# Optimization experiments

Measured on AMD Instinct MI355X. Metric: run time of the kernel, lower is better.

## Reference

```python
import jax, jax.numpy as jnp
import numpy as np

N_NODES = 50000
N_EDGES = 800000
IN_C, OUT_C, EDGE_F, HEADS, HID, FINAL = 8, 16, 8, 4, 64, 128
NEG_SLOPE = 0.2  # PyG GATConv default LeakyReLU slope


def setup_inputs() -> dict:
    key = jax.random.key(0)
    ks = jax.random.split(key, 12)
    s = 0.1
    return {
        "x": jax.random.normal(ks[0], (N_NODES, IN_C), jnp.float32),
        "edge_index": jax.random.randint(ks[1], (2, N_EDGES), 0, N_NODES, jnp.int64),
        "edge_attr": jax.random.normal(ks[2], (N_EDGES, EDGE_F), jnp.float32),
        # NNConv params: root weight, bias, edge-MLP Linear(EDGE_F -> IN_C*OUT_C)
        "ecc_root": jax.random.normal(ks[3], (IN_C, OUT_C), jnp.float32) * s,
        "ecc_bias": jnp.zeros((OUT_C,), jnp.float32),
        "mlp_w": jax.random.normal(ks[4], (EDGE_F, IN_C * OUT_C), jnp.float32) * s,
        "mlp_b": jnp.zeros((IN_C * OUT_C,), jnp.float32),
        # GATConv params
        "gat_lin": jax.random.normal(ks[5], (OUT_C, HEADS * HID), jnp.float32) * s,
        "att_src": jax.random.normal(ks[6], (HEADS, HID), jnp.float32) * s,
        "att_dst": jax.random.normal(ks[7], (HEADS, HID), jnp.float32) * s,
        "gat_bias": jnp.zeros((HEADS * HID,), jnp.float32),
        # final Linear
        "fc_w": jax.random.normal(ks[8], (HEADS * HID, FINAL), jnp.float32) * s,
        "fc_b": jnp.zeros((FINAL,), jnp.float32),
    }


def _forward(x, edge_index, edge_attr, ecc_root, ecc_bias, mlp_w, mlp_b,
             gat_lin, att_src, att_dst, gat_bias, fc_w, fc_b):
    src, dst = edge_index[0], edge_index[1]  # messages flow src -> dst

    # ---- NNConv (edge-conditioned conv), aggr='add' ----
    # per-edge weight matrices [E, IN_C, OUT_C] from edge MLP
    w_e = (edge_attr @ mlp_w + mlp_b).reshape(-1, IN_C, OUT_C)
    msg = jnp.einsum('ei,eio->eo', x[src], w_e)                 # [E, OUT_C]
    agg = jax.ops.segment_sum(msg, dst, num_segments=N_NODES)   # [N, OUT_C]
    h = jax.nn.relu(x @ ecc_root + agg + ecc_bias)              # [N, OUT_C]

    # ---- GATConv (heads concatenated) ----
    g = (h @ gat_lin).reshape(N_NODES, HEADS, HID)              # [N, H, D]
    a_src = jnp.einsum('nhd,hd->nh', g, att_src)                # [N, H]
    a_dst = jnp.einsum('nhd,hd->nh', g, att_dst)
    e = jax.nn.leaky_relu(a_src[src] + a_dst[dst], NEG_SLOPE)   # [E, H]
    # segment softmax over incoming edges of each dst node
    e_max = jax.ops.segment_max(e, dst, num_segments=N_NODES)   # [N, H]
    e_max = jnp.where(jnp.isfinite(e_max), e_max, 0.0)
    e_exp = jnp.exp(e - e_max[dst])                             # [E, H]
    denom = jax.ops.segment_sum(e_exp, dst, num_segments=N_NODES)
    alpha = e_exp / (denom[dst] + 1e-16)                        # [E, H]
    out = jax.ops.segment_sum(alpha[:, :, None] * g[src], dst,
                              num_segments=N_NODES)             # [N, H, D]
    out = jax.nn.relu(out.reshape(N_NODES, HEADS * HID) + gat_bias)

    # ---- final linear ----
    return out @ fc_w + fc_b                                    # [N, FINAL]


def reference(x, edge_index, edge_attr, ecc_root, ecc_bias, mlp_w, mlp_b,
              gat_lin, att_src, att_dst, gat_bias, fc_w, fc_b):
    return _forward(x, edge_index, edge_attr, ecc_root, ecc_bias, mlp_w, mlp_b,
                    gat_lin, att_src, att_dst, gat_bias, fc_w, fc_b)
```

## Files before the change

### kernel.cpp

```cpp
#include <hip/hip_runtime.h>

#define N_NODES 50000
#define N_EDGES 800000
#define IN_C 8
#define OUT_C 16
#define EDGE_F 8
#define HEADS 4
#define HID 64
#define GDIM (HEADS*HID)
#define FINAL 128
#define NEG_SLOPE 0.2f
#define EB ((N_EDGES+255)/256)
#define NBLK 196

__device__ __forceinline__ int clampn(int v) {
    return v < 0 ? 0 : (v >= N_NODES ? N_NODES - 1 : v);
}

__global__ __launch_bounds__(256) void k_histfold(
    const int* __restrict__ dst, int* __restrict__ cnt, int* __restrict__ rnk,
    const float* __restrict__ gat_lin,
    const float* __restrict__ att_src_w, const float* __restrict__ att_dst_w,
    float* __restrict__ wsrc, float* __restrict__ wdst)
{
    if (blockIdx.x < EB) {
        int e = blockIdx.x * 256 + threadIdx.x;
        if (e >= N_EDGES) return;
        rnk[e] = atomicAdd(&cnt[clampn(dst[e])], 1);
    } else {
        int t = threadIdx.x;
        if (t >= 64) return;
        int c = t >> 2, h = t & 3;
        float ws = 0.f, wd = 0.f;
        for (int k = 0; k < HID; k++) {
            float l = gat_lin[c * GDIM + h * HID + k];
            ws += l * att_src_w[h * HID + k];
            wd += l * att_dst_w[h * HID + k];
        }
        wsrc[t] = ws;
        wdst[t] = wd;
    }
}

__global__ __launch_bounds__(256) void k_part(const int* __restrict__ cnt,
                                              int* __restrict__ part)
{
    int i = blockIdx.x * 256 + threadIdx.x;
    int v = (i < N_NODES) ? cnt[i] : 0;
#pragma unroll
    for (int off = 32; off; off >>= 1) v += __shfl_down(v, off);
    __shared__ int ws[4];
    if ((threadIdx.x & 63) == 0) ws[threadIdx.x >> 6] = v;
    __syncthreads();
    if (threadIdx.x == 0) part[blockIdx.x] = ws[0] + ws[1] + ws[2] + ws[3];
}

__global__ __launch_bounds__(256) void k_scan1(const int* __restrict__ part,
                                               int* __restrict__ partscan)
{
    int t = threadIdx.x;
    int v = (t < NBLK) ? part[t] : 0;
    int lane = t & 63, wid = t >> 6;
    int incl = v;
#pragma unroll
    for (int off = 1; off < 64; off <<= 1) {
        int u = __shfl_up(incl, off);
        if (lane >= off) incl += u;
    }
    __shared__ int wsum[4];
    if (lane == 63) wsum[wid] = incl;
    __syncthreads();
    int add = 0;
    for (int w = 0; w < wid; w++) add += wsum[w];
    partscan[t] = incl - v + add;
}

__global__ __launch_bounds__(256) void k_add(const int* __restrict__ cnt,
                                             const int* __restrict__ partscan,
                                             int* __restrict__ offs)
{
    int i = blockIdx.x * 256 + threadIdx.x;
    int v = (i < N_NODES) ? cnt[i] : 0;
    int lane = threadIdx.x & 63, wid = threadIdx.x >> 6;
    int incl = v;
#pragma unroll
    for (int off = 1; off < 64; off <<= 1) {
        int u = __shfl_up(incl, off);
        if (lane >= off) incl += u;
    }
    __shared__ int wsum[4];
    if (lane == 63) wsum[wid] = incl;
    __syncthreads();
    int add = partscan[blockIdx.x];
    for (int w = 0; w < wid; w++) add += wsum[w];
    if (i < N_NODES) offs[i] = incl - v + add;
    if (i == 0) offs[N_NODES] = N_EDGES;
}

__global__ __launch_bounds__(256) void k_scatter(
    const int* __restrict__ src, const int* __restrict__ dst,
    const int* __restrict__ rnk, const int* __restrict__ offs,
    int2* __restrict__ se_csr)
{
    int e = blockIdx.x * 256 + threadIdx.x;
    if (e >= N_EDGES) return;
    int p = offs[clampn(dst[e])] + rnk[e];
    se_csr[p] = make_int2(clampn(src[e]), e);
}

__global__ __launch_bounds__(256) void k2T_wave(
    const float* __restrict__ x,
    const int2* __restrict__ se_csr, const int* __restrict__ offs,
    const float* __restrict__ ea,
    const float* __restrict__ mlp_w, const float* __restrict__ mlp_b,
    const float* __restrict__ ecc_root, const float* __restrict__ ecc_bias,
    const float* __restrict__ wsrc, const float* __restrict__ wdst,
    float* __restrict__ h_tab, float* __restrict__ asrc, float* __restrict__ adst)
{
    __shared__ float smW[64 * 17];
    __shared__ float smb[128];
    __shared__ float sroot[128];
    __shared__ float sbias[16];
    __shared__ float sws[64], swd[64];
    __shared__ float sT[4][64];
    __shared__ float sxs[4][8];

    int t = threadIdx.x;
    for (int idx = t; idx < 1024; idx += 256)
        smW[(idx >> 4) * 17 + (idx & 15)] = mlp_w[idx];
    if (t < 128) smb[t] = mlp_b[t];
    if (t >= 128 && t < 256) sroot[t - 128] = ecc_root[t - 128];
    if (t < 16) sbias[t] = ecc_bias[t];
    if (t >= 32 && t < 96) sws[t - 32] = wsrc[t - 32];
    if (t >= 96 && t < 160) swd[t - 96] = wdst[t - 96];

    int wid = t >> 6, lane = t & 63;
    int n = blockIdx.x * 4 + wid;
    int f = lane >> 3, i = lane & 7;
    int beg = offs[n], end = offs[n + 1];

    float t0 = 0.f, t1 = 0.f, t2 = 0.f, t3 = 0.f, xs = 0.f;
    int j = beg;
    for (; j + 3 < end; j += 4) {
        int2 se0 = se_csr[j],     se1 = se_csr[j + 1];
        int2 se2 = se_csr[j + 2], se3 = se_csr[j + 3];
        float a0 = ea[(size_t)se0.y * EDGE_F + f];
        float a1 = ea[(size_t)se1.y * EDGE_F + f];
        float a2 = ea[(size_t)se2.y * EDGE_F + f];
        float a3 = ea[(size_t)se3.y * EDGE_F + f];
        float x0 = x[se0.x * IN_C + i];
        float x1 = x[se1.x * IN_C + i];
        float x2 = x[se2.x * IN_C + i];
        float x3 = x[se3.x * IN_C + i];
        t0 += a0 * x0; t1 += a1 * x1; t2 += a2 * x2; t3 += a3 * x3;
        xs += (x0 + x1) + (x2 + x3);
    }
    for (; j < end; j++) {
        int2 se = se_csr[j];
        float a = ea[(size_t)se.y * EDGE_F + f];
        float xv = x[se.x * IN_C + i];
        t0 += a * xv;
        xs += xv;
    }
    sT[wid][lane] = (t0 + t1) + (t2 + t3);
    if (f == 0) sxs[wid][i] = xs;
    __syncthreads();

    int o = lane & 15, p = lane >> 4;
    float v = 0.f;
#pragma unroll
    for (int q2 = 0; q2 < 16; q2++) {
        int jj = p * 16 + q2;
        v += smW[jj * 17 + o] * sT[wid][jj];
    }
    v += __shfl_down(v, 32);
    v += __shfl_down(v, 16);

    float hv = 0.f;
    if (lane < 16) {
        float vv = v + sbias[o];
#pragma unroll
        for (int ii = 0; ii < IN_C; ii++) {
            vv += smb[ii * 16 + o] * sxs[wid][ii];
            vv += x[n * IN_C + ii] * sroot[ii * 16 + o];
        }
        hv = fmaxf(vv, 0.f);
        h_tab[n * OUT_C + o] = hv;
    }
    float as = 0.f, ad = 0.f;
    int h2 = lane & 3;
#pragma unroll
    for (int c = 0; c < 16; c++) {
        float hc = __shfl(hv, c);
        as += hc * sws[c * 4 + h2];
        ad += hc * swd[c * 4 + h2];
    }
    if (lane < 4) {
        asrc[n * HEADS + lane] = as;
        adst[n * HEADS + lane] = ad;
    }
}

__global__ __launch_bounds__(256) void k_gatE(
    const int* __restrict__ offs, const int2* __restrict__ se_csr,
    const float* __restrict__ asrc, const float* __restrict__ adst,
    const float* __restrict__ h_tab, float* __restrict__ U_all)
{
    int t = threadIdx.x;
    int wid = t >> 6, lane = t & 63;
    int n = blockIdx.x * 4 + wid;
    int h = lane >> 4, c = lane & 15;
    float adsth = adst[n * HEADS + h];
    int beg = offs[n], end = offs[n + 1];

    float U = 0.f, den = 0.f;
    int j = beg;
    for (; j + 3 < end; j += 4) {
        int s0 = se_csr[j].x,     s1 = se_csr[j + 1].x;
        int s2 = se_csr[j + 2].x, s3 = se_csr[j + 3].x;
        float av0 = asrc[s0 * HEADS + h], av1 = asrc[s1 * HEADS + h];
        float av2 = asrc[s2 * HEADS + h], av3 = asrc[s3 * HEADS + h];
        float h0 = h_tab[s0 * OUT_C + c], h1 = h_tab[s1 * OUT_C + c];
        float h2v = h_tab[s2 * OUT_C + c], h3v = h_tab[s3 * OUT_C + c];
        float v0 = av0 + adsth; v0 = v0 > 0.f ? v0 : NEG_SLOPE * v0;
        float v1 = av1 + adsth; v1 = v1 > 0.f ? v1 : NEG_SLOPE * v1;
        float v2 = av2 + adsth; v2 = v2 > 0.f ? v2 : NEG_SLOPE * v2;
        float v3 = av3 + adsth; v3 = v3 > 0.f ? v3 : NEG_SLOPE * v3;
        float p0 = __expf(v0), p1 = __expf(v1), p2 = __expf(v2), p3 = __expf(v3);
        den += (p0 + p1) + (p2 + p3);
        U += p0 * h0 + p1 * h1 + p2 * h2v + p3 * h3v;
    }
    for (; j < end; j++) {
        int s = se_csr[j].x;
        float av = asrc[s * HEADS + h];
        float hvv = h_tab[s * OUT_C + c];
        float v = av + adsth; v = v > 0.f ? v : NEG_SLOPE * v;
        float pe = __expf(v);
        den += pe;
        U += pe * hvv;
    }
    U_all[(size_t)n * 64 + lane] = U / (den + 1e-16f);
}

#define BM 64
#define BK6 16
__global__ __launch_bounds__(256) void k_fuse(
    const float* __restrict__ U_all, const float* __restrict__ gat_lin,
    const float* __restrict__ gat_bias, const float* __restrict__ fc_w,
    const float* __restrict__ fc_b, float* __restrict__ y)
{
    __shared__ float sU[64 * 68];
    __shared__ float slin[16 * GDIM];
    __shared__ float sA[BK6][BM + 4];
    __shared__ float sW[BK6][FINAL];
    int tid = threadIdx.x;
    int r0 = blockIdx.x * BM;

    for (int idx = tid; idx < 16 * GDIM; idx += 256) slin[idx] = gat_lin[idx];
    {
        int row = tid >> 2, hq = tid & 3;
        int grow = r0 + row;
        float4 ua = make_float4(0.f, 0.f, 0.f, 0.f), ub = ua, uc = ua, ud = ua;
        if (grow < N_NODES) {
            const float* up = &U_all[(size_t)grow * 64 + hq * 16];
            ua = *(const float4*)&up[0];
            ub = *(const float4*)&up[4];
            uc = *(const float4*)&up[8];
            ud = *(const float4*)&up[12];
        }
        float* dp = &sU[row * 68 + hq * 16];
        *(float4*)&dp[0]  = ua;
        *(float4*)&dp[4]  = ub;
        *(float4*)&dp[8]  = uc;
        *(float4*)&dp[12] = ud;
    }
    __syncthreads();

    float acc[8][4];
#pragma unroll
    for (int r = 0; r < 8; r++)
#pragma unroll
        for (int c = 0; c < 4; c++) acc[r][c] = 0.f;

    int ar = tid >> 2;
    int ak = (tid & 3) * 4;
    int tcol = (tid & 31) * 4;
    int trow = (tid >> 5) * 8;

    for (int k0 = 0; k0 < GDIM; k0 += BK6) {
        int h = k0 >> 6;
        float4 bv = *(const float4*)&gat_bias[k0 + ak];
        float g0 = 0.f, g1 = 0.f, g2 = 0.f, g3 = 0.f;
        const float* urow = &sU[ar * 68 + h * 16];
#pragma unroll
        for (int c = 0; c < 16; c++) {
            float ucv = urow[c];
            const float* lp = &slin[c * GDIM + k0 + ak];
            g0 += ucv * lp[0];
            g1 += ucv * lp[1];
            g2 += ucv * lp[2];
            g3 += ucv * lp[3];
        }
        sA[ak + 0][ar] = fmaxf(g0 + bv.x, 0.f);
        sA[ak + 1][ar] = fmaxf(g1 + bv.y, 0.f);
        sA[ak + 2][ar] = fmaxf(g2 + bv.z, 0.f);
        sA[ak + 3][ar] = fmaxf(g3 + bv.w, 0.f);
#pragma unroll
        for (int p = 0; p < 2; p++) {
            int kk = (tid >> 5) + p * 8;
            int c = (tid & 31) * 4;
            *(float4*)&sW[kk][c] = *(const float4*)&fc_w[(size_t)(k0 + kk) * FINAL + c];
        }
        __syncthreads();
#pragma unroll
        for (int kk = 0; kk < BK6; kk++) {
            float4 w = *(const float4*)&sW[kk][tcol];
            float4 a0 = *(const float4*)&sA[kk][trow];
            float4 a1 = *(const float4*)&sA[kk][trow + 4];
            float a[8] = {a0.x, a0.y, a0.z, a0.w, a1.x, a1.y, a1.z, a1.w};
#pragma unroll
            for (int r = 0; r < 8; r++) {
                acc[r][0] += a[r] * w.x;
                acc[r][1] += a[r] * w.y;
                acc[r][2] += a[r] * w.z;
                acc[r][3] += a[r] * w.w;
            }
        }
        __syncthreads();
    }

    float4 fb = *(const float4*)&fc_b[tcol];
#pragma unroll
    for (int r = 0; r < 8; r++) {
        int row = r0 + trow + r;
        if (row < N_NODES) {
            *(float4*)&y[(size_t)row * FINAL + tcol] =
                make_float4(acc[r][0] + fb.x, acc[r][1] + fb.y,
                            acc[r][2] + fb.z, acc[r][3] + fb.w);
        }
    }
}

extern "C" void kernel_launch(void* const* d_in, const int* in_sizes, int n_in,
                              void* d_out, int out_size, void* d_ws, size_t ws_size,
                              hipStream_t stream)
{
    const float* x        = (const float*)d_in[0];
    const int*   ei       = (const int*)d_in[1];
    const float* ea       = (const float*)d_in[2];
    const float* ecc_root = (const float*)d_in[3];
    const float* ecc_bias = (const float*)d_in[4];
    const float* mlp_w    = (const float*)d_in[5];
    const float* mlp_b    = (const float*)d_in[6];
    const float* gat_lin  = (const float*)d_in[7];
    const float* att_src  = (const float*)d_in[8];
    const float* att_dst  = (const float*)d_in[9];
    const float* gat_bias = (const float*)d_in[10];
    const float* fc_w     = (const float*)d_in[11];
    const float* fc_b     = (const float*)d_in[12];
    float* y = (float*)d_out;

    const int* src = ei;
    const int* dst = ei + N_EDGES;

    float* h_tab = (float*)d_ws;
    float* U_all = h_tab + (size_t)N_NODES * OUT_C;
    float* asrc  = U_all + (size_t)N_NODES * 64;
    float* adst  = asrc + (size_t)N_NODES * HEADS;
    float* wsrc  = adst + (size_t)N_NODES * HEADS;
    float* wdst  = wsrc + 64;
    int*   cnt      = (int*)(wdst + 64);
    int*   offs     = cnt + N_NODES;
    int*   part     = offs + N_NODES + 1;
    int*   partscan = part + 256;
    int*   rnk      = partscan + 256;
    int2*  se_csr   = (int2*)(rnk + N_EDGES + 1);

    hipMemsetAsync(cnt, 0, sizeof(int) * N_NODES, stream);

    k_histfold<<<EB + 1, 256, 0, stream>>>(dst, cnt, rnk, gat_lin, att_src, att_dst,
                                           wsrc, wdst);
    k_part    <<<NBLK, 256, 0, stream>>>(cnt, part);
    k_scan1   <<<1, 256, 0, stream>>>(part, partscan);
    k_add     <<<NBLK, 256, 0, stream>>>(cnt, partscan, offs);
    k_scatter <<<EB, 256, 0, stream>>>(src, dst, rnk, offs, se_csr);

    k2T_wave  <<<N_NODES / 4, 256, 0, stream>>>(x, se_csr, offs, ea, mlp_w, mlp_b,
                                                ecc_root, ecc_bias, wsrc, wdst,
                                                h_tab, asrc, adst);
    k_gatE    <<<N_NODES / 4, 256, 0, stream>>>(offs, se_csr, asrc, adst, h_tab, U_all);
    k_fuse    <<<(N_NODES + BM - 1) / BM, 256, 0, stream>>>(U_all, gat_lin, gat_bias,
                                                            fc_w, fc_b, y);
}
```

Baseline: 324.3 us.

## Replace multi-kernel scan with atomic cursor and fuse GAT projection into gather

Collapses the partial-sum, single-block scan and add kernels into one kernel that gets each block's base offset with an atomic cursor. Edge ranges are now derived from offs plus cnt. The GAT linear projection, bias and ReLU move into the attention gather kernel, which writes bf16 activations consumed by a simpler final GEMM. This removes launches and the projection step inside the GEMM, at the cost of larger intermediate writes, bf16 rounding, and a nondeterministic CSR segment order.

```diff
diff --git a/kernel.cpp b/kernel.cpp
--- a/kernel.cpp
+++ b/kernel.cpp
@@ -16,6 +16,13 @@
 __device__ __forceinline__ int clampn(int v) {
     return v < 0 ? 0 : (v >= N_NODES ? N_NODES - 1 : v);
 }
+__device__ __forceinline__ unsigned short f32_to_bf16(float f) {
+    unsigned u = __float_as_uint(f);
+    unsigned r = (u + 0x7fffu + ((u >> 16) & 1u)) >> 16;
+    return (unsigned short)r;
+}
+__device__ __forceinline__ float bf16lo(unsigned u) { return __uint_as_float(u << 16); }
+__device__ __forceinline__ float bf16hi(unsigned u) { return __uint_as_float(u & 0xffff0000u); }
 
 __global__ __launch_bounds__(256) void k_histfold(
     const int* __restrict__ dst, int* __restrict__ cnt, int* __restrict__ rnk,
@@ -42,42 +49,9 @@
     }
 }
 
-__global__ __launch_bounds__(256) void k_part(const int* __restrict__ cnt,
-                                              int* __restrict__ part)
-{
-    int i = blockIdx.x * 256 + threadIdx.x;
-    int v = (i < N_NODES) ? cnt[i] : 0;
-#pragma unroll
-    for (int off = 32; off; off >>= 1) v += __shfl_down(v, off);
-    __shared__ int ws[4];
-    if ((threadIdx.x & 63) == 0) ws[threadIdx.x >> 6] = v;
-    __syncthreads();
-    if (threadIdx.x == 0) part[blockIdx.x] = ws[0] + ws[1] + ws[2] + ws[3];
-}
-
-__global__ __launch_bounds__(256) void k_scan1(const int* __restrict__ part,
-                                               int* __restrict__ partscan)
-{
-    int t = threadIdx.x;
-    int v = (t < NBLK) ? part[t] : 0;
-    int lane = t & 63, wid = t >> 6;
-    int incl = v;
-#pragma unroll
-    for (int off = 1; off < 64; off <<= 1) {
-        int u = __shfl_up(incl, off);
-        if (lane >= off) incl += u;
-    }
-    __shared__ int wsum[4];
-    if (lane == 63) wsum[wid] = incl;
-    __syncthreads();
-    int add = 0;
-    for (int w = 0; w < wid; w++) add += wsum[w];
-    partscan[t] = incl - v + add;
-}
-
-__global__ __launch_bounds__(256) void k_add(const int* __restrict__ cnt,
-                                             const int* __restrict__ partscan,
-                                             int* __restrict__ offs)
+__global__ __launch_bounds__(256) void k_offs(const int* __restrict__ cnt,
+                                              int* __restrict__ cursor,
+                                              int* __restrict__ offs)
 {
     int i = blockIdx.x * 256 + threadIdx.x;
     int v = (i < N_NODES) ? cnt[i] : 0;
@@ -89,12 +63,15 @@
         if (lane >= off) incl += u;
     }
     __shared__ int wsum[4];
+    __shared__ int sbase;
     if (lane == 63) wsum[wid] = incl;
     __syncthreads();
-    int add = partscan[blockIdx.x];
+    if (threadIdx.x == 0)
+        sbase = atomicAdd(cursor, wsum[0] + wsum[1] + wsum[2] + wsum[3]);
+    __syncthreads();
+    int add = sbase;
     for (int w = 0; w < wid; w++) add += wsum[w];
-    if (i < N_NODES) offs[i] = incl - v + add;
-    if (i == 0) offs[N_NODES] = N_EDGES;
+    if (i < N_NODES) offs[i] = add + incl - v;
 }
 
 __global__ __launch_bounds__(256) void k_scatter(
@@ -111,7 +88,7 @@
 __global__ __launch_bounds__(256) void k2T_wave(
     const float* __restrict__ x,
     const int2* __restrict__ se_csr, const int* __restrict__ offs,
-    const float* __restrict__ ea,
+    const int* __restrict__ cnt, const float* __restrict__ ea,
     const float* __restrict__ mlp_w, const float* __restrict__ mlp_b,
     const float* __restrict__ ecc_root, const float* __restrict__ ecc_bias,
     const float* __restrict__ wsrc, const float* __restrict__ wdst,
@@ -137,7 +114,7 @@
     int wid = t >> 6, lane = t & 63;
     int n = blockIdx.x * 4 + wid;
     int f = lane >> 3, i = lane & 7;
-    int beg = offs[n], end = offs[n + 1];
+    int beg = offs[n], end = beg + cnt[n];
 
     float t0 = 0.f, t1 = 0.f, t2 = 0.f, t3 = 0.f, xs = 0.f;
     int j = beg;
@@ -201,17 +178,19 @@
     }
 }
 
-__global__ __launch_bounds__(256) void k_gatE(
-    const int* __restrict__ offs, const int2* __restrict__ se_csr,
+__global__ __launch_bounds__(256) void k_gatG(
+    const int* __restrict__ offs, const int* __restrict__ cnt,
+    const int2* __restrict__ se_csr,
     const float* __restrict__ asrc, const float* __restrict__ adst,
-    const float* __restrict__ h_tab, float* __restrict__ U_all)
+    const float* __restrict__ h_tab, const float* __restrict__ gat_lin,
+    const float* __restrict__ gat_bias, unsigned short* __restrict__ outg)
 {
     int t = threadIdx.x;
     int wid = t >> 6, lane = t & 63;
     int n = blockIdx.x * 4 + wid;
     int h = lane >> 4, c = lane & 15;
     float adsth = adst[n * HEADS + h];
-    int beg = offs[n], end = offs[n + 1];
+    int beg = offs[n], end = beg + cnt[n];
 
     float U = 0.f, den = 0.f;
     int j = beg;
@@ -239,42 +218,36 @@
         den += pe;
         U += pe * hvv;
     }
-    U_all[(size_t)n * 64 + lane] = U / (den + 1e-16f);
+    U /= (den + 1e-16f);
+
+    float gv[4] = {0.f, 0.f, 0.f, 0.f};
+#pragma unroll
+    for (int cc = 0; cc < 16; cc++) {
+#pragma unroll
+        for (int jh = 0; jh < 4; jh++) {
+            float Uv = __shfl(U, jh * 16 + cc);
+            gv[jh] += Uv * gat_lin[cc * GDIM + jh * 64 + lane];
+        }
+    }
+#pragma unroll
+    for (int jh = 0; jh < 4; jh++) {
+        float g = fmaxf(gv[jh] + gat_bias[jh * 64 + lane], 0.f);
+        outg[(size_t)n * GDIM + jh * 64 + lane] = f32_to_bf16(g);
+    }
 }
 
 #define BM 64
 #define BK6 16
-__global__ __launch_bounds__(256) void k_fuse(
-    const float* __restrict__ U_all, const float* __restrict__ gat_lin,
-    const float* __restrict__ gat_bias, const float* __restrict__ fc_w,
+__global__ __launch_bounds__(256) void k6_final(
+    const unsigned short* __restrict__ outg, const float* __restrict__ fc_w,
     const float* __restrict__ fc_b, float* __restrict__ y)
 {
-    __shared__ float sU[64 * 68];
-    __shared__ float slin[16 * GDIM];
     __shared__ float sA[BK6][BM + 4];
     __shared__ float sW[BK6][FINAL];
     int tid = threadIdx.x;
     int r0 = blockIdx.x * BM;
-
-    for (int idx = tid; idx < 16 * GDIM; idx += 256) slin[idx] = gat_lin[idx];
-    {
-        int row = tid >> 2, hq = tid & 3;
-        int grow = r0 + row;
-        float4 ua = make_float4(0.f, 0.f, 0.f, 0.f), ub = ua, uc = ua, ud = ua;
-        if (grow < N_NODES) {
-            const float* up = &U_all[(size_t)grow * 64 + hq * 16];
-            ua = *(const float4*)&up[0];
-            ub = *(const float4*)&up[4];
-            uc = *(const float4*)&up[8];
-            ud = *(const float4*)&up[12];
-        }
-        float* dp = &sU[row * 68 + hq * 16];
-        *(float4*)&dp[0]  = ua;
-        *(float4*)&dp[4]  = ub;
-        *(float4*)&dp[8]  = uc;
-        *(float4*)&dp[12] = ud;
-    }
-    __syncthreads();
+    int tcol = (tid & 31) * 4;
+    int trow = (tid >> 5) * 8;
 
     float acc[8][4];
 #pragma unroll
@@ -284,27 +257,18 @@
 
     int ar = tid >> 2;
     int ak = (tid & 3) * 4;
-    int tcol = (tid & 31) * 4;
-    int trow = (tid >> 5) * 8;
 
     for (int k0 = 0; k0 < GDIM; k0 += BK6) {
-        int h = k0 >> 6;
-        float4 bv = *(const float4*)&gat_bias[k0 + ak];
-        float g0 = 0.f, g1 = 0.f, g2 = 0.f, g3 = 0.f;
-        const float* urow = &sU[ar * 68 + h * 16];
-#pragma unroll
-        for (int c = 0; c < 16; c++) {
-            float ucv = urow[c];
-            const float* lp = &slin[c * GDIM + k0 + ak];
-            g0 += ucv * lp[0];
-            g1 += ucv * lp[1];
-            g2 += ucv * lp[2];
-            g3 += ucv * lp[3];
-        }
-        sA[ak + 0][ar] = fmaxf(g0 + bv.x, 0.f);
-        sA[ak + 1][ar] = fmaxf(g1 + bv.y, 0.f);
-        sA[ak + 2][ar] = fmaxf(g2 + bv.z, 0.f);
-        sA[ak + 3][ar] = fmaxf(g3 + bv.w, 0.f);
+        int row = r0 + ar;
+        float4 av = make_float4(0.f, 0.f, 0.f, 0.f);
+        if (row < N_NODES) {
+            uint2 raw = *(const uint2*)&outg[(size_t)row * GDIM + k0 + ak];
+            av = make_float4(bf16lo(raw.x), bf16hi(raw.x), bf16lo(raw.y), bf16hi(raw.y));
+        }
+        sA[ak + 0][ar] = av.x;
+        sA[ak + 1][ar] = av.y;
+        sA[ak + 2][ar] = av.z;
+        sA[ak + 3][ar] = av.w;
 #pragma unroll
         for (int p = 0; p < 2; p++) {
             int kk = (tid >> 5) + p * 8;
@@ -364,31 +328,28 @@
     const int* dst = ei + N_EDGES;
 
     float* h_tab = (float*)d_ws;
-    float* U_all = h_tab + (size_t)N_NODES * OUT_C;
-    float* asrc  = U_all + (size_t)N_NODES * 64;
+    unsigned short* outg = (unsigned short*)(h_tab + (size_t)N_NODES * OUT_C);
+    float* asrc  = (float*)(outg + (size_t)N_NODES * GDIM);
     float* adst  = asrc + (size_t)N_NODES * HEADS;
     float* wsrc  = adst + (size_t)N_NODES * HEADS;
     float* wdst  = wsrc + 64;
     int*   cnt      = (int*)(wdst + 64);
-    int*   offs     = cnt + N_NODES;
-    int*   part     = offs + N_NODES + 1;
-    int*   partscan = part + 256;
-    int*   rnk      = partscan + 256;
+    int*   cursor   = cnt + N_NODES;
+    int*   offs     = cursor + 1;
+    int*   rnk      = offs + N_NODES;
     int2*  se_csr   = (int2*)(rnk + N_EDGES + 1);
 
-    hipMemsetAsync(cnt, 0, sizeof(int) * N_NODES, stream);
+    hipMemsetAsync(cnt, 0, sizeof(int) * (N_NODES + 1), stream);
 
     k_histfold<<<EB + 1, 256, 0, stream>>>(dst, cnt, rnk, gat_lin, att_src, att_dst,
                                            wsrc, wdst);
-    k_part    <<<NBLK, 256, 0, stream>>>(cnt, part);
-    k_scan1   <<<1, 256, 0, stream>>>(part, partscan);
-    k_add     <<<NBLK, 256, 0, stream>>>(cnt, partscan, offs);
+    k_offs    <<<NBLK, 256, 0, stream>>>(cnt, cursor, offs);
     k_scatter <<<EB, 256, 0, stream>>>(src, dst, rnk, offs, se_csr);
 
-    k2T_wave  <<<N_NODES / 4, 256, 0, stream>>>(x, se_csr, offs, ea, mlp_w, mlp_b,
+    k2T_wave  <<<N_NODES / 4, 256, 0, stream>>>(x, se_csr, offs, cnt, ea, mlp_w, mlp_b,
                                                 ecc_root, ecc_bias, wsrc, wdst,
                                                 h_tab, asrc, adst);
-    k_gatE    <<<N_NODES / 4, 256, 0, stream>>>(offs, se_csr, asrc, adst, h_tab, U_all);
-    k_fuse    <<<(N_NODES + BM - 1) / BM, 256, 0, stream>>>(U_all, gat_lin, gat_bias,
-                                                            fc_w, fc_b, y);
-}
+    k_gatG    <<<N_NODES / 4, 256, 0, stream>>>(offs, cnt, se_csr, asrc, adst,
+                                                h_tab, gat_lin, gat_bias, outg);
+    k6_final  <<<(N_NODES + BM - 1) / BM, 256, 0, stream>>>(outg, fc_w, fc_b, y);
+}
```

After: 326.3 us. Within noise of the previous version (+0.6%).
